# Kernel tuning notes

Hardware: AMD Instinct MI355X
Metric: run time of the kernel (lower is better)

## Reference

```python
import jax, jax.numpy as jnp
import numpy as np

D = 512; H = 8; DFF = 2048; S1 = 1024; S2 = 512; B = 8; EPS = 1e-5


def setup_inputs() -> dict:
    key = jax.random.key(0)
    ks = jax.random.split(key, 10)
    def w(k, shape):
        return jax.random.normal(k, shape, dtype=jnp.float32) * 0.02
    return {
        "rna_embed": jax.random.normal(ks[0], (S1, B, D), dtype=jnp.float32),
        "protein_embed": jax.random.normal(ks[1], (S2, B, D), dtype=jnp.float32),
        # self-attention params (torch MHA packed in_proj)
        "Wqkv_s": w(ks[2], (3 * D, D)), "bqkv_s": jnp.zeros((3 * D,), jnp.float32),
        "Wo_s": w(ks[3], (D, D)), "bo_s": jnp.zeros((D,), jnp.float32),
        # cross-attention params
        "Wqkv_c": w(ks[4], (3 * D, D)), "bqkv_c": jnp.zeros((3 * D,), jnp.float32),
        "Wo_c": w(ks[5], (D, D)), "bo_c": jnp.zeros((D,), jnp.float32),
        # FFN params
        "W1": w(ks[6], (DFF, D)), "b1": jnp.zeros((DFF,), jnp.float32),
        "W2": w(ks[7], (D, DFF)), "b2": jnp.zeros((D,), jnp.float32),
        # LayerNorm params: norm0_1, norm1_1, norm1_2, norm2
        "g0": jnp.ones((D,), jnp.float32), "be0": jnp.zeros((D,), jnp.float32),
        "g11": jnp.ones((D,), jnp.float32), "be11": jnp.zeros((D,), jnp.float32),
        "g12": jnp.ones((D,), jnp.float32), "be12": jnp.zeros((D,), jnp.float32),
        "g2": jnp.ones((D,), jnp.float32), "be2": jnp.zeros((D,), jnp.float32),
    }


def _layernorm(x, g, b):
    m = jnp.mean(x, axis=-1, keepdims=True)
    v = jnp.mean(jnp.square(x - m), axis=-1, keepdims=True)
    return (x - m) * jax.lax.rsqrt(v + EPS) * g + b


def _mha(xq, xkv, Wqkv, bqkv, Wo, bo):
    # xq: (Sq, B, D), xkv: (Sk, B, D)
    Wq, Wk, Wv = jnp.split(Wqkv, 3, axis=0)
    bq, bk, bv = jnp.split(bqkv, 3)
    hd = D // H
    scale = 1.0 / np.sqrt(hd).astype(np.float32)
    q = (xq @ Wq.T + bq).reshape(xq.shape[0], -1, H, hd)   # (Sq,B,H,hd)
    k = (xkv @ Wk.T + bk).reshape(xkv.shape[0], -1, H, hd)  # (Sk,B,H,hd)
    v = (xkv @ Wv.T + bv).reshape(xkv.shape[0], -1, H, hd)
    scores = jnp.einsum('qbhd,kbhd->bhqk', q, k) * scale    # (B,H,Sq,Sk)
    attn = jax.nn.softmax(scores, axis=-1)
    o = jnp.einsum('bhqk,kbhd->qbhd', attn, v).reshape(xq.shape[0], -1, D)
    return o @ Wo.T + bo


def reference(rna_embed, protein_embed, Wqkv_s, bqkv_s, Wo_s, bo_s,
              Wqkv_c, bqkv_c, Wo_c, bo_c, W1, b1, W2, b2,
              g0, be0, g11, be11, g12, be12, g2, be2):
    x1 = rna_embed
    # pre-norm self-attention
    h = _layernorm(x1, g0, be0)
    x1 = x1 + _mha(h, h, Wqkv_s, bqkv_s, Wo_s, bo_s)
    # pre-norm cross-attention (queries from x1, keys/values from protein)
    x1 = x1 + _mha(_layernorm(x1, g11, be11), _layernorm(protein_embed, g12, be12),
                   Wqkv_c, bqkv_c, Wo_c, bo_c)
    # pre-norm FFN
    h = _layernorm(x1, g2, be2)
    x1 = x1 + (jax.nn.relu(h @ W1.T + b1) @ W2.T + b2)
    return x1
```

## Files before the change

### kernel.cpp

```cpp
#include <hip/hip_runtime.h>

typedef unsigned short u16;
typedef unsigned int u32;
typedef u16 u16x8 __attribute__((ext_vector_type(8)));
typedef u16 u16x4 __attribute__((ext_vector_type(4)));
typedef short bfx8 __attribute__((ext_vector_type(8)));
typedef float f32x4 __attribute__((ext_vector_type(4)));

#define AS1 __attribute__((address_space(1)))
#define AS3 __attribute__((address_space(3)))

__device__ __forceinline__ u16 f2bf(float f) {
  union { float f; u32 u; } c; c.f = f;
  u32 u = c.u;
  u += 0x7fffu + ((u >> 16) & 1u);
  return (u16)(u >> 16);
}

__device__ __forceinline__ float bf2f(u16 b) {
  union { u32 u; float f; } c; c.u = ((u32)b) << 16;
  return c.f;
}

__device__ __forceinline__ u32 cvt_pk_bf16(float lo, float hi) {
  u32 r;
  asm("v_cvt_pk_bf16_f32 %0, %1, %2" : "=v"(r) : "v"(lo), "v"(hi));
  return r;
}

__device__ __forceinline__ float fexp2(float x) {
  float r;
  asm("v_exp_f32 %0, %1" : "=v"(r) : "v"(x));
  return r;
}

__device__ __forceinline__ void ln_core(float f[8], const float* __restrict__ g,
                                        const float* __restrict__ be,
                                        u16* __restrict__ out, int gw, int lane) {
  float s = 0.f, q = 0.f;
#pragma unroll
  for (int e = 0; e < 8; ++e) { s += f[e]; q += f[e] * f[e]; }
#pragma unroll
  for (int m = 1; m < 64; m <<= 1) { s += __shfl_xor(s, m); q += __shfl_xor(q, m); }
  float mean = s * (1.f / 512.f);
  float var = q * (1.f / 512.f) - mean * mean;
  float rs = rsqrtf(var + 1e-5f);
  const float4* g4 = (const float4*)g;
  const float4* b4 = (const float4*)be;
  float4 ga = g4[2 * lane], gb = g4[2 * lane + 1];
  float4 ba = b4[2 * lane], bb = b4[2 * lane + 1];
  float gv[8] = {ga.x, ga.y, ga.z, ga.w, gb.x, gb.y, gb.z, gb.w};
  float bv[8] = {ba.x, ba.y, ba.z, ba.w, bb.x, bb.y, bb.z, bb.w};
  u16x8 o;
#pragma unroll
  for (int e = 0; e < 8; ++e) o[e] = f2bf((f[e] - mean) * rs * gv[e] + bv[e]);
  ((u16x8*)(out + (size_t)gw * 512))[lane] = o;
}

__device__ __forceinline__ void ln_row_f32(const float* __restrict__ x, const float* __restrict__ g,
                                           const float* __restrict__ be, u16* __restrict__ out,
                                           int gw, int lane) {
  const float4* row = (const float4*)(x + (size_t)gw * 512);
  float4 a = row[2 * lane], b = row[2 * lane + 1];
  float f[8] = {a.x, a.y, a.z, a.w, b.x, b.y, b.z, b.w};
  ln_core(f, g, be, out, gw, lane);
}

__device__ __forceinline__ void ln_row_bf16(const u16* __restrict__ x, const float* __restrict__ g,
                                            const float* __restrict__ be, u16* __restrict__ out,
                                            int gw, int lane) {
  u16x8 v = ((const u16x8*)(x + (size_t)gw * 512))[lane];
  float f[8];
#pragma unroll
  for (int e = 0; e < 8; ++e) f[e] = bf2f(v[e]);
  ln_core(f, g, be, out, gw, lane);
}

__global__ __launch_bounds__(256) void cvtln_kernel(const float* __restrict__ a0, const float* __restrict__ a1,
                                                    const float* __restrict__ a2, const float* __restrict__ a3,
                                                    const float* __restrict__ a4, const float* __restrict__ a5,
                                                    u16* __restrict__ b0, u16* __restrict__ b1,
                                                    u16* __restrict__ b2, u16* __restrict__ b3,
                                                    u16* __restrict__ b4, u16* __restrict__ b5,
                                                    const float* __restrict__ x, const float* __restrict__ g,
                                                    const float* __restrict__ be, u16* __restrict__ lnout) {
  if (blockIdx.x < 4096) {
    int i = blockIdx.x * 256 + threadIdx.x;
    const float* s; u16* d; int off;
    if      (i < 196608) { s = a0; d = b0; off = i; }
    else if (i < 262144) { s = a1; d = b1; off = i - 196608; }
    else if (i < 458752) { s = a2; d = b2; off = i - 262144; }
    else if (i < 524288) { s = a3; d = b3; off = i - 458752; }
    else if (i < 786432) { s = a4; d = b4; off = i - 524288; }
    else                 { s = a5; d = b5; off = i - 786432; }
    float4 v = ((const float4*)s)[off];
    u16x4 o;
    o[0] = f2bf(v.x); o[1] = f2bf(v.y); o[2] = f2bf(v.z); o[3] = f2bf(v.w);
    ((u16x4*)d)[off] = o;
  } else {
    int gw = ((blockIdx.x - 4096) * 256 + threadIdx.x) >> 6;
    ln_row_f32(x, g, be, lnout, gw, threadIdx.x & 63);
  }
}

__global__ __launch_bounds__(256) void lnb_kernel(const u16* __restrict__ x,
                                                  const float* __restrict__ g,
                                                  const float* __restrict__ be,
                                                  u16* __restrict__ out, int ntok) {
  int gw = (blockIdx.x * 256 + threadIdx.x) >> 6;
  if (gw >= ntok) return;
  ln_row_bf16(x, g, be, out, gw, threadIdx.x & 63);
}

__global__ __launch_bounds__(256) void ln2_kernel(const u16* __restrict__ xa, const float* __restrict__ ga,
                                                  const float* __restrict__ ba, u16* __restrict__ oa,
                                                  const float* __restrict__ xb, const float* __restrict__ gb,
                                                  const float* __restrict__ bb, u16* __restrict__ ob) {
  int lane = threadIdx.x & 63;
  if (blockIdx.x < 2048) {
    int gw = (blockIdx.x * 256 + threadIdx.x) >> 6;
    ln_row_bf16(xa, ga, ba, oa, gw, lane);
  } else {
    int gw = ((blockIdx.x - 2048) * 256 + threadIdx.x) >> 6;
    ln_row_f32(xb, gb, bb, ob, gw, lane);
  }
}

__global__ __launch_bounds__(256) void vt_kernel(const u16* __restrict__ vB, u16* __restrict__ vt,
                                                 int stride, int S) {
  __shared__ u16 lt[64 * 68];
  const int t = threadIdx.x;
  const int b = blockIdx.y, h = blockIdx.z;
  const int sr = t >> 3, dc = (t & 7) * 8;
#pragma unroll
  for (int p = 0; p < 2; ++p) {
    int s = blockIdx.x * 64 + sr + p * 32;
    u16x8 v = *(const u16x8*)(vB + (size_t)(s * 8 + b) * stride + h * 64 + dc);
    u16x4 lo, hi;
    lo[0]=v[0]; lo[1]=v[1]; lo[2]=v[2]; lo[3]=v[3];
    hi[0]=v[4]; hi[1]=v[5]; hi[2]=v[6]; hi[3]=v[7];
    *(u16x4*)&lt[(sr + p * 32) * 68 + dc] = lo;
    *(u16x4*)&lt[(sr + p * 32) * 68 + dc + 4] = hi;
  }
  __syncthreads();
#pragma unroll
  for (int p = 0; p < 2; ++p) {
    int d = sr + p * 32;
    u16x8 o;
#pragma unroll
    for (int e = 0; e < 8; ++e) o[e] = lt[(dc + e) * 68 + d];
    *(u16x8*)(vt + ((size_t)(b * 8 + h) * 64 + d) * S + blockIdx.x * 64 + dc) = o;
  }
}

template <int EPI, int BM, int BN>
__device__ __forceinline__ void gemm8_body(const u16* __restrict__ A,
                                           const u16* __restrict__ Bw,
                                           const float* __restrict__ bias,
                                           const void* __restrict__ res,
                                           void* __restrict__ Cout,
                                           int M, int K, int bn, int bm) {
  constexpr int WCg = BN / 64;
  constexpr int WRg = 8 / WCg;
  constexpr int RPW = BM / WRg;
  constexpr int IM = RPW / 16;
  constexpr int LD = (BM + BN) / 64;
  __shared__ __align__(16) u16 lA[2][BM * 64];
  __shared__ __align__(16) u16 lB[2][BN * 64];
  const int tid = threadIdx.x;
  const int lane = tid & 63, w = tid >> 6;
  const int wr = w / WCg, wc = w % WCg;
  const int r15 = lane & 15, kg = lane >> 4;
  const int xr = (r15 & 7) << 4;

  f32x4 acc[IM][4] = {};

  const int lrw = tid >> 3;
  const int lcl = ((tid & 7) * 8) ^ ((lrw & 7) * 8);
  const u16* gA = A + (size_t)(bn + lrw) * K + lcl;
  const u16* gB = Bw + (size_t)(bm + lrw) * K + lcl;
  const int ldsbase = (w * 8) * 64;

#define STAGE8(buf, t) do {                                                               \
    _Pragma("unroll")                                                                     \
    for (int i_ = 0; i_ < BM / 64; ++i_)                                                  \
      __builtin_amdgcn_global_load_lds((AS1 u32*)(gA + (size_t)(i_ * 64) * K + (t) * 64), \
                                       (AS3 u32*)&lA[buf][i_ * 4096 + ldsbase], 16, 0, 0);\
    _Pragma("unroll")                                                                     \
    for (int i_ = 0; i_ < BN / 64; ++i_)                                                  \
      __builtin_amdgcn_global_load_lds((AS1 u32*)(gB + (size_t)(i_ * 64) * K + (t) * 64), \
                                       (AS3 u32*)&lB[buf][i_ * 4096 + ldsbase], 16, 0, 0);\
  } while (0)

  const int nk = K >> 6;
  STAGE8(0, 0);
  for (int t = 0; t < nk; ++t) {
    const int cur = t & 1;
    if (t + 1 < nk) {
      STAGE8(cur ^ 1, t + 1);
      if constexpr (LD == 3)      asm volatile("s_waitcnt vmcnt(3)" ::: "memory");
      else if constexpr (LD == 4) asm volatile("s_waitcnt vmcnt(4)" ::: "memory");
      else                        asm volatile("s_waitcnt vmcnt(8)" ::: "memory");
    } else {
      asm volatile("s_waitcnt vmcnt(0)" ::: "memory");
    }
    __builtin_amdgcn_sched_barrier(0);
    __builtin_amdgcn_s_barrier();
    __builtin_amdgcn_sched_barrier(0);

    const char* Ac = (const char*)lA[cur];
    const char* Bc = (const char*)lB[cur];
    __builtin_amdgcn_s_setprio(1);
#pragma unroll
    for (int kk = 0; kk < 2; ++kk) {
      bfx8 a[IM], b[4];
#pragma unroll
      for (int i = 0; i < IM; ++i)
        a[i] = *(const bfx8*)(Ac + (wr * RPW + i * 16 + r15) * 128 + ((kk * 64 + kg * 16) ^ xr));
#pragma unroll
      for (int j = 0; j < 4; ++j)
        b[j] = *(const bfx8*)(Bc + (wc * 64 + j * 16 + r15) * 128 + ((kk * 64 + kg * 16) ^ xr));
#pragma unroll
      for (int i = 0; i < IM; ++i)
#pragma unroll
        for (int j = 0; j < 4; ++j)
          acc[i][j] = __builtin_amdgcn_mfma_f32_16x16x32_bf16(a[i], b[j], acc[i][j], 0, 0, 0);
    }
    __builtin_amdgcn_s_setprio(0);
    __builtin_amdgcn_sched_barrier(0);
    __builtin_amdgcn_s_barrier();
  }
#undef STAGE8

#pragma unroll
  for (int i = 0; i < IM; ++i) {
#pragma unroll
    for (int j = 0; j < 4; ++j) {
      int col = bm + wc * 64 + j * 16 + r15;
      float bv = bias[col];
#pragma unroll
      for (int r = 0; r < 4; ++r) {
        int row = bn + wr * RPW + i * 16 + kg * 4 + r;
        size_t idx = (size_t)row * M + col;
        float v = acc[i][j][r] + bv;
        if (EPI == 1) v = fmaxf(v, 0.f);
        if (EPI == 3) {
          ((u16*)Cout)[idx] = f2bf(((const float*)res)[idx] + v);
        } else if (EPI == 4) {
          ((u16*)Cout)[idx] = f2bf(bf2f(((const u16*)res)[idx]) + v);
        } else if (EPI == 5) {
          ((float*)Cout)[idx] = bf2f(((const u16*)res)[idx]) + v;
        } else {
          ((u16*)Cout)[idx] = f2bf(v);
        }
      }
    }
  }
}

template <int EPI, int BM, int BN, int MINW>
__global__ __launch_bounds__(512, MINW) void gemm8(const u16* __restrict__ A,
                                                   const u16* __restrict__ Bw,
                                                   const float* __restrict__ bias,
                                                   const void* __restrict__ res,
                                                   void* __restrict__ Cout,
                                                   int N, int M, int K) {
  const int nwg = gridDim.x * gridDim.y;
  const int id = blockIdx.y * gridDim.x + blockIdx.x;
  const int swz = (id & 7) * (nwg >> 3) + (id >> 3);
  const int bn = (swz / gridDim.x) * BM;
  const int bm = (swz % gridDim.x) * BN;
  gemm8_body<EPI, BM, BN>(A, Bw, bias, res, Cout, M, K, bn, bm);
}

__global__ __launch_bounds__(512, 6) void gemm8_dual(const u16* __restrict__ A0, const u16* __restrict__ W0,
                                                     const float* __restrict__ c0, u16* __restrict__ O0,
                                                     const u16* __restrict__ A1, const u16* __restrict__ W1,
                                                     const float* __restrict__ c1, u16* __restrict__ O1) {
  const int id = blockIdx.x;
  const u16 *A, *Bw; const float* bias; u16* C; int M, gx, lid;
  if (id < 512) { A = A0; Bw = W0; bias = c0; C = O0; M = 512;  gx = 4; lid = id; }
  else          { A = A1; Bw = W1; bias = c1; C = O1; M = 1024; gx = 8; lid = id - 512; }
  const int swz = (lid & 7) * 64 + (lid >> 3);
  const int bn = (swz / gx) * 64;
  const int bm = (swz % gx) * 128;
  gemm8_body<0, 64, 128>(A, Bw, bias, nullptr, C, M, 512, bn, bm);
}

__global__ __launch_bounds__(512, 4) void attn_kernel(const u16* __restrict__ qB,
                                                      const u16* __restrict__ kB,
                                                      const u16* __restrict__ vtB,
                                                      u16* __restrict__ oB,
                                                      int qStride, int kvStride, int Sk) {
  __shared__ __align__(16) u16 lK[4][64 * 64];
  __shared__ __align__(16) u16 lVt[4][64 * 64];
  __shared__ __align__(16) u16 lP[8][16 * 64];
  const int tid = threadIdx.x, lane = tid & 63, w = tid >> 6;
  const int sid = blockIdx.x;
  const int h = sid & 7, b = (sid >> 3) & 7, qt = sid >> 6;
  const int r15 = lane & 15, kg = lane >> 4;
  const int srow = lane >> 3;
  const int sxcol = ((lane & 7) * 8) ^ (srow * 8);

  const int qs = qt * 128 + w * 16 + r15;
  const u16* qrow = qB + (size_t)(qs * 8 + b) * qStride + h * 64;
  bfx8 qf0 = *(const bfx8*)(qrow + kg * 8);
  bfx8 qf1 = *(const bfx8*)(qrow + 32 + kg * 8);

  const u16* vbase = vtB + ((size_t)(b * 8 + h) * 64) * Sk;
  const u16* kp0 = kB + ((size_t)(w * 8 + srow) * 8 + b) * kvStride + h * 64 + sxcol;
  const size_t kAdv = (size_t)64 * 8 * kvStride;
  const u16* vp0 = vbase + (size_t)(w * 8 + srow) * Sk + sxcol;

#define STAGE(buf, tt) do {                                                           \
    __builtin_amdgcn_global_load_lds((AS1 u32*)(kp0 + (size_t)(tt) * kAdv),           \
                                     (AS3 u32*)&lK[buf][(w * 8) * 64], 16, 0, 0);     \
    __builtin_amdgcn_global_load_lds((AS1 u32*)(vp0 + (size_t)(tt) * 64),             \
                                     (AS3 u32*)&lVt[buf][(w * 8) * 64], 16, 0, 0);    \
  } while (0)

  const int nt = Sk / 64;
  const int np = nt >> 1;
  STAGE(0, 0); STAGE(1, 1);

  f32x4 oacc[4] = {};
  float mrow = -1e30f, lsum = 0.f;
  const float C2 = 0.125f * 1.44269504088896340736f;
  const int xr = (r15 & 7) << 4;
  char* myP = (char*)lP[w];

  for (int i = 0; i < np; ++i) {
    const int ba = (i & 1) * 2, bb = ba + 1;
    __builtin_amdgcn_sched_barrier(0);
    __builtin_amdgcn_s_barrier();
    __builtin_amdgcn_sched_barrier(0);
    if (i + 1 < np) {
      const int sb = ((i + 1) & 1) * 2;
      STAGE(sb, 2 * (i + 1)); STAGE(sb + 1, 2 * (i + 1) + 1);
      asm volatile("s_waitcnt vmcnt(4)" ::: "memory");
    } else {
      asm volatile("s_waitcnt vmcnt(0)" ::: "memory");
    }
    __builtin_amdgcn_sched_barrier(0);

    const char* Ka = (const char*)lK[ba];
    const char* Kb = (const char*)lK[bb];
    f32x4 sa[4] = {}, sb_[4] = {};
    __builtin_amdgcn_s_setprio(1);
#pragma unroll
    for (int j = 0; j < 4; ++j) {
      const char* kpa = Ka + (j * 16 + r15) * 128;
      bfx8 ka0 = *(const bfx8*)(kpa + ((kg * 16) ^ xr));
      bfx8 ka1 = *(const bfx8*)(kpa + ((64 + kg * 16) ^ xr));
      sa[j] = __builtin_amdgcn_mfma_f32_16x16x32_bf16(ka0, qf0, sa[j], 0, 0, 0);
      sa[j] = __builtin_amdgcn_mfma_f32_16x16x32_bf16(ka1, qf1, sa[j], 0, 0, 0);
    }
#pragma unroll
    for (int j = 0; j < 4; ++j) {
      const char* kpb = Kb + (j * 16 + r15) * 128;
      bfx8 kb0 = *(const bfx8*)(kpb + ((kg * 16) ^ xr));
      bfx8 kb1 = *(const bfx8*)(kpb + ((64 + kg * 16) ^ xr));
      sb_[j] = __builtin_amdgcn_mfma_f32_16x16x32_bf16(kb0, qf0, sb_[j], 0, 0, 0);
      sb_[j] = __builtin_amdgcn_mfma_f32_16x16x32_bf16(kb1, qf1, sb_[j], 0, 0, 0);
    }
    __builtin_amdgcn_s_setprio(0);

    float lm = fmaxf(fmaxf(fmaxf(sa[0][0], sa[0][1]), fmaxf(sa[0][2], sa[0][3])),
              fmaxf(fmaxf(fmaxf(sa[1][0], sa[1][1]), fmaxf(sa[1][2], sa[1][3])),
              fmaxf(fmaxf(fmaxf(sa[2][0], sa[2][1]), fmaxf(sa[2][2], sa[2][3])),
                    fmaxf(fmaxf(sa[3][0], sa[3][1]), fmaxf(sa[3][2], sa[3][3])))));
    float lmb = fmaxf(fmaxf(fmaxf(sb_[0][0], sb_[0][1]), fmaxf(sb_[0][2], sb_[0][3])),
               fmaxf(fmaxf(fmaxf(sb_[1][0], sb_[1][1]), fmaxf(sb_[1][2], sb_[1][3])),
               fmaxf(fmaxf(fmaxf(sb_[2][0], sb_[2][1]), fmaxf(sb_[2][2], sb_[2][3])),
                     fmaxf(fmaxf(sb_[3][0], sb_[3][1]), fmaxf(sb_[3][2], sb_[3][3])))));
    lm = fmaxf(lm, lmb);

    if (!__all(lm <= mrow + 16.0f)) {
      float m0 = fmaxf(lm, __shfl_xor(lm, 16));
      m0 = fmaxf(m0, __shfl_xor(m0, 32));
      float mn = fmaxf(mrow, m0);
      float corr = fexp2((mrow - mn) * C2);
      mrow = mn;
      lsum *= corr;
#pragma unroll
      for (int jd = 0; jd < 4; ++jd)
#pragma unroll
        for (int r = 0; r < 4; ++r) oacc[jd][r] *= corr;
    }
    float bc = -mrow * C2;

    float pa[4][4], pb[4][4];
#pragma unroll
    for (int j = 0; j < 4; ++j)
#pragma unroll
      for (int r = 0; r < 4; ++r) {
        pa[j][r] = fexp2(fmaf(sa[j][r], C2, bc));
        pb[j][r] = fexp2(fmaf(sb_[j][r], C2, bc));
      }
    float ps = 0.f;
#pragma unroll
    for (int j = 0; j < 4; ++j)
#pragma unroll
      for (int r = 0; r < 4; ++r) ps += pa[j][r] + pb[j][r];
    lsum += ps;

#pragma unroll
    for (int j = 0; j < 4; ++j)
#pragma unroll
      for (int h2 = 0; h2 < 2; ++h2) {
        u32 pk = cvt_pk_bf16(pa[j][2 * h2], pa[j][2 * h2 + 1]);
        int k0b = (j * 16 + kg * 4 + 2 * h2) * 2;
        *(u32*)(myP + r15 * 128 + (k0b ^ xr)) = pk;
      }
    const char* Va = (const char*)lVt[ba];
    __builtin_amdgcn_s_setprio(1);
#pragma unroll
    for (int s2 = 0; s2 < 2; ++s2) {
      bfx8 ptf = *(const bfx8*)(myP + r15 * 128 + ((s2 * 64 + kg * 16) ^ xr));
#pragma unroll
      for (int jd = 0; jd < 4; ++jd) {
        const char* vp = Va + (jd * 16 + r15) * 128;
        bfx8 vf = *(const bfx8*)(vp + ((s2 * 64 + kg * 16) ^ xr));
        oacc[jd] = __builtin_amdgcn_mfma_f32_16x16x32_bf16(vf, ptf, oacc[jd], 0, 0, 0);
      }
    }
    __builtin_amdgcn_s_setprio(0);

#pragma unroll
    for (int j = 0; j < 4; ++j)
#pragma unroll
      for (int h2 = 0; h2 < 2; ++h2) {
        u32 pk = cvt_pk_bf16(pb[j][2 * h2], pb[j][2 * h2 + 1]);
        int k0b = (j * 16 + kg * 4 + 2 * h2) * 2;
        *(u32*)(myP + r15 * 128 + (k0b ^ xr)) = pk;
      }
    const char* Vb = (const char*)lVt[bb];
    __builtin_amdgcn_s_setprio(1);
#pragma unroll
    for (int s2 = 0; s2 < 2; ++s2) {
      bfx8 ptf = *(const bfx8*)(myP + r15 * 128 + ((s2 * 64 + kg * 16) ^ xr));
#pragma unroll
      for (int jd = 0; jd < 4; ++jd) {
        const char* vp = Vb + (jd * 16 + r15) * 128;
        bfx8 vf = *(const bfx8*)(vp + ((s2 * 64 + kg * 16) ^ xr));
        oacc[jd] = __builtin_amdgcn_mfma_f32_16x16x32_bf16(vf, ptf, oacc[jd], 0, 0, 0);
      }
    }
    __builtin_amdgcn_s_setprio(0);
  }
#undef STAGE

  lsum += __shfl_xor(lsum, 16);
  lsum += __shfl_xor(lsum, 32);
  float inv = 1.f / lsum;
  const int s = qt * 128 + w * 16 + r15;
  u16* orow = oB + (size_t)(s * 8 + b) * 512 + h * 64;
#pragma unroll
  for (int jd = 0; jd < 4; ++jd) {
    u32 p0 = cvt_pk_bf16(oacc[jd][0] * inv, oacc[jd][1] * inv);
    u32 p1 = cvt_pk_bf16(oacc[jd][2] * inv, oacc[jd][3] * inv);
    *(u32*)(orow + jd * 16 + kg * 4) = p0;
    *(u32*)(orow + jd * 16 + kg * 4 + 2) = p1;
  }
}

extern "C" void kernel_launch(void* const* d_in, const int* in_sizes, int n_in,
                              void* d_out, int out_size, void* d_ws, size_t ws_size,
                              hipStream_t stream) {
  const float* rna    = (const float*)d_in[0];
  const float* prot   = (const float*)d_in[1];
  const float* Wqkv_s = (const float*)d_in[2];
  const float* bqkv_s = (const float*)d_in[3];
  const float* Wo_s   = (const float*)d_in[4];
  const float* bo_s   = (const float*)d_in[5];
  const float* Wqkv_c = (const float*)d_in[6];
  const float* bqkv_c = (const float*)d_in[7];
  const float* Wo_c   = (const float*)d_in[8];
  const float* bo_c   = (const float*)d_in[9];
  const float* W1     = (const float*)d_in[10];
  const float* b1     = (const float*)d_in[11];
  const float* W2     = (const float*)d_in[12];
  const float* b2     = (const float*)d_in[13];
  const float* g0  = (const float*)d_in[14];
  const float* be0 = (const float*)d_in[15];
  const float* g11 = (const float*)d_in[16];
  const float* be11= (const float*)d_in[17];
  const float* g12 = (const float*)d_in[18];
  const float* be12= (const float*)d_in[19];
  const float* g2  = (const float*)d_in[20];
  const float* be2 = (const float*)d_in[21];
  float* out = (float*)d_out;

  u16* wbf      = (u16*)d_ws;
  u16* w_qkv_s  = wbf;
  u16* w_o_s    = wbf + 786432;
  u16* w_qkv_c  = wbf + 1048576;
  u16* w_o_c    = wbf + 1835008;
  u16* w_1      = wbf + 2097152;
  u16* w_2      = wbf + 3145728;
  u16* hbuf     = wbf + 4194304;
  u16* qkv      = hbuf + 4194304;
  u16* kvc      = qkv + 4194304;
  u16* attnO    = qkv + 12582912;
  u16* hp       = attnO + 4194304;
  u16* x1b      = hp + 2097152;
  u16* x1c      = x1b + 4194304;
  u16* ffnmid   = qkv;

  cvtln_kernel<<<6144, 256, 0, stream>>>(Wqkv_s, Wo_s, Wqkv_c, Wo_c, W1, W2,
                                         w_qkv_s, w_o_s, w_qkv_c, w_o_c, w_1, w_2,
                                         rna, g0, be0, hbuf);

  gemm8<0, 128, 128, 4><<<dim3(12, 64), 512, 0, stream>>>(hbuf, w_qkv_s, bqkv_s, nullptr, qkv, 8192, 1536, 512);
  vt_kernel<<<dim3(16, 8, 8), 256, 0, stream>>>(qkv + 1024, hbuf, 1536, 1024);
  attn_kernel<<<512, 512, 0, stream>>>(qkv, qkv + 512, hbuf, attnO, 1536, 1536, 1024);
  gemm8<3, 64, 128, 6><<<dim3(4, 128), 512, 0, stream>>>(attnO, w_o_s, bo_s, rna, x1b, 8192, 512, 512);

  ln2_kernel<<<3072, 256, 0, stream>>>(x1b, g11, be11, hbuf, prot, g12, be12, hp);
  gemm8_dual<<<1024, 512, 0, stream>>>(hbuf, w_qkv_c, bqkv_c, qkv,
                                       hp, w_qkv_c + 512 * 512, bqkv_c + 512, kvc);
  vt_kernel<<<dim3(8, 8, 8), 256, 0, stream>>>(kvc + 512, hp, 1024, 512);
  attn_kernel<<<512, 512, 0, stream>>>(qkv, kvc, hp, attnO, 512, 1024, 512);
  gemm8<4, 64, 128, 6><<<dim3(4, 128), 512, 0, stream>>>(attnO, w_o_c, bo_c, x1b, x1c, 8192, 512, 512);

  lnb_kernel<<<2048, 256, 0, stream>>>(x1c, g2, be2, hbuf, 8192);
  gemm8<1, 256, 256, 2><<<dim3(8, 32), 512, 0, stream>>>(hbuf, w_1, b1, nullptr, ffnmid, 8192, 2048, 512);
  gemm8<5, 64, 128, 6><<<dim3(4, 128), 512, 0, stream>>>(ffnmid, w_2, b2, x1c, out, 8192, 512, 2048);
}
```

Measured before the change: 191.5 us.

## Keep softmax probabilities in registers by permuting K rows to match MFMA layout

Removes the per-wave LDS scratch used to transpose the probability tile between the QK^T and PV MFMAs. K rows are loaded into LDS in a permuted order so the score accumulator layout already matches the B-operand layout of the PV MFMA, and P is packed directly from registers. This drops LDS writes and reads plus 16KB of shared memory per block, which may raise occupancy. Correctness depends on the row permutation exactly matching the register layout.

```diff
diff --git a/kernel.cpp b/kernel.cpp
--- a/kernel.cpp
+++ b/kernel.cpp
@@ -294,7 +294,6 @@
                                                       int qStride, int kvStride, int Sk) {
   __shared__ __align__(16) u16 lK[4][64 * 64];
   __shared__ __align__(16) u16 lVt[4][64 * 64];
-  __shared__ __align__(16) u16 lP[8][16 * 64];
   const int tid = threadIdx.x, lane = tid & 63, w = tid >> 6;
   const int sid = blockIdx.x;
   const int h = sid & 7, b = (sid >> 3) & 7, qt = sid >> 6;
@@ -307,10 +306,13 @@
   bfx8 qf0 = *(const bfx8*)(qrow + kg * 8);
   bfx8 qf1 = *(const bfx8*)(qrow + 32 + kg * 8);
 
+  const int rl = w * 8 + srow;
+  const int krow = (rl & 32) | ((rl & 12) << 1) | ((rl & 16) >> 2) | (rl & 3);
+
   const u16* vbase = vtB + ((size_t)(b * 8 + h) * 64) * Sk;
-  const u16* kp0 = kB + ((size_t)(w * 8 + srow) * 8 + b) * kvStride + h * 64 + sxcol;
+  const u16* kp0 = kB + ((size_t)krow * 8 + b) * kvStride + h * 64 + sxcol;
   const size_t kAdv = (size_t)64 * 8 * kvStride;
-  const u16* vp0 = vbase + (size_t)(w * 8 + srow) * Sk + sxcol;
+  const u16* vp0 = vbase + (size_t)rl * Sk + sxcol;
 
 #define STAGE(buf, tt) do {                                                           \
     __builtin_amdgcn_global_load_lds((AS1 u32*)(kp0 + (size_t)(tt) * kAdv),           \
@@ -327,7 +329,6 @@
   float mrow = -1e30f, lsum = 0.f;
   const float C2 = 0.125f * 1.44269504088896340736f;
   const int xr = (r15 & 7) << 4;
-  char* myP = (char*)lP[w];
 
   for (int i = 0; i < np; ++i) {
     const int ba = (i & 1) * 2, bb = ba + 1;
@@ -404,46 +405,38 @@
       for (int r = 0; r < 4; ++r) ps += pa[j][r] + pb[j][r];
     lsum += ps;
 
-#pragma unroll
-    for (int j = 0; j < 4; ++j)
-#pragma unroll
-      for (int h2 = 0; h2 < 2; ++h2) {
-        u32 pk = cvt_pk_bf16(pa[j][2 * h2], pa[j][2 * h2 + 1]);
-        int k0b = (j * 16 + kg * 4 + 2 * h2) * 2;
-        *(u32*)(myP + r15 * 128 + (k0b ^ xr)) = pk;
-      }
     const char* Va = (const char*)lVt[ba];
     __builtin_amdgcn_s_setprio(1);
 #pragma unroll
     for (int s2 = 0; s2 < 2; ++s2) {
-      bfx8 ptf = *(const bfx8*)(myP + r15 * 128 + ((s2 * 64 + kg * 16) ^ xr));
+      union { u32 u[4]; bfx8 v; } pt;
+      pt.u[0] = cvt_pk_bf16(pa[2 * s2][0],     pa[2 * s2][1]);
+      pt.u[1] = cvt_pk_bf16(pa[2 * s2][2],     pa[2 * s2][3]);
+      pt.u[2] = cvt_pk_bf16(pa[2 * s2 + 1][0], pa[2 * s2 + 1][1]);
+      pt.u[3] = cvt_pk_bf16(pa[2 * s2 + 1][2], pa[2 * s2 + 1][3]);
 #pragma unroll
       for (int jd = 0; jd < 4; ++jd) {
         const char* vp = Va + (jd * 16 + r15) * 128;
         bfx8 vf = *(const bfx8*)(vp + ((s2 * 64 + kg * 16) ^ xr));
-        oacc[jd] = __builtin_amdgcn_mfma_f32_16x16x32_bf16(vf, ptf, oacc[jd], 0, 0, 0);
+        oacc[jd] = __builtin_amdgcn_mfma_f32_16x16x32_bf16(vf, pt.v, oacc[jd], 0, 0, 0);
       }
     }
     __builtin_amdgcn_s_setprio(0);
 
-#pragma unroll
-    for (int j = 0; j < 4; ++j)
-#pragma unroll
-      for (int h2 = 0; h2 < 2; ++h2) {
-        u32 pk = cvt_pk_bf16(pb[j][2 * h2], pb[j][2 * h2 + 1]);
-        int k0b = (j * 16 + kg * 4 + 2 * h2) * 2;
-        *(u32*)(myP + r15 * 128 + (k0b ^ xr)) = pk;
-      }
     const char* Vb = (const char*)lVt[bb];
     __builtin_amdgcn_s_setprio(1);
 #pragma unroll
     for (int s2 = 0; s2 < 2; ++s2) {
-      bfx8 ptf = *(const bfx8*)(myP + r15 * 128 + ((s2 * 64 + kg * 16) ^ xr));
+      union { u32 u[4]; bfx8 v; } pt;
+      pt.u[0] = cvt_pk_bf16(pb[2 * s2][0],     pb[2 * s2][1]);
+      pt.u[1] = cvt_pk_bf16(pb[2 * s2][2],     pb[2 * s2][3]);
+      pt.u[2] = cvt_pk_bf16(pb[2 * s2 + 1][0], pb[2 * s2 + 1][1]);
+      pt.u[3] = cvt_pk_bf16(pb[2 * s2 + 1][2], pb[2 * s2 + 1][3]);
 #pragma unroll
       for (int jd = 0; jd < 4; ++jd) {
         const char* vp = Vb + (jd * 16 + r15) * 128;
         bfx8 vf = *(const bfx8*)(vp + ((s2 * 64 + kg * 16) ^ xr));
-        oacc[jd] = __builtin_amdgcn_mfma_f32_16x16x32_bf16(vf, ptf, oacc[jd], 0, 0, 0);
+        oacc[jd] = __builtin_amdgcn_mfma_f32_16x16x32_bf16(vf, pt.v, oacc[jd], 0, 0, 0);
       }
     }
     __builtin_amdgcn_s_setprio(0);
```

Result: no change. 188.0 us (-1.9%).
